# Performance work log

Hardware: AMD Instinct MI355X
Metric: run time of the kernel (lower is better)

## Reference

```python
import jax, jax.numpy as jnp
import numpy as np

COMMITMENT_COST = 0.25


def setup_inputs() -> dict:
    key = jax.random.key(0)
    k1, k2 = jax.random.split(key)
    x = jax.random.normal(k1, (65536, 256), dtype=jnp.float32)
    codebook = jax.random.normal(k2, (1024, 256), dtype=jnp.float32)
    return {"x": x, "codebook": codebook}


def reference(x, codebook):
    # Flatten to [N, D] (already 2D here).
    flat = x.reshape(-1, codebook.shape[1])
    # Squared euclidean distances [N, K]; argmin matches torch.cdist argmin.
    x2 = jnp.sum(flat * flat, axis=1, keepdims=True)          # [N, 1]
    c2 = jnp.sum(codebook * codebook, axis=1)                  # [K]
    d2 = x2 - 2.0 * (flat @ codebook.T) + c2[None, :]          # [N, K]
    encoding_indices = jnp.argmin(d2, axis=1)                  # [N]
    quantized = codebook[encoding_indices]                     # [N, D]
    # VQ loss + commitment loss
    vq_loss = jnp.mean((jax.lax.stop_gradient(quantized) - flat) ** 2)
    commitment_loss = jnp.mean((quantized - jax.lax.stop_gradient(flat)) ** 2)
    quantization_loss = vq_loss + COMMITMENT_COST * commitment_loss
    # Straight-through estimator
    quantized_st = flat + jax.lax.stop_gradient(quantized - flat)
    quantized_st = quantized_st.reshape(x.shape)
    return quantized_st, quantization_loss, encoding_indices
```

## Files before the change

kernel.cpp:

```cpp
#include <hip/hip_runtime.h>

#define NROWS 65536
#define DDIM  256
#define KCODES 1024
#define MARGIN 0.05f
#define TIE_WINDOW 8.0e-5
#define FLAGCAP 8192

typedef __attribute__((ext_vector_type(8))) short bf16x8;
typedef __attribute__((ext_vector_type(4))) float f32x4;

union F4 { float4 v; float f[4]; };

__device__ __forceinline__ unsigned bf16rne(float f) {
    unsigned u = __float_as_uint(f);
    return (u + 0x7fffu + ((u >> 16) & 1u)) >> 16;
}
__device__ __forceinline__ float bf16tof(unsigned h) {
    return __uint_as_float(h << 16);
}

__global__ __launch_bounds__(64) void c2_kernel(const float* __restrict__ cb,
                                                float* __restrict__ c2f,
                                                double* __restrict__ c2d,
                                                int* __restrict__ cnt) {
    const int c = blockIdx.x, lane = threadIdx.x;
    if (c == 0 && lane == 0) cnt[0] = 0;
    F4 v; v.v = reinterpret_cast<const float4*>(cb + (size_t)c * DDIM)[lane];
    double s = (double)v.f[0] * v.f[0] + (double)v.f[1] * v.f[1]
             + (double)v.f[2] * v.f[2] + (double)v.f[3] * v.f[3];
    #pragma unroll
    for (int off = 32; off; off >>= 1) s += __shfl_xor(s, off);
    if (lane == 0) { c2d[c] = s; c2f[c] = (float)s; }
}

__global__ __launch_bounds__(256) void prep_frags(const float* __restrict__ cb,
                                                  unsigned short* __restrict__ fh,
                                                  unsigned short* __restrict__ fl) {
    int t = blockIdx.x * 256 + threadIdx.x;
    int j0   = (t & 1) * 4;
    int lane = (t >> 1) & 63;
    int ks   = (t >> 7) & 7;
    int ntg  = t >> 10;
    int c = ntg * 16 + (lane & 15);
    int k = ks * 32 + (lane >> 4) * 8 + j0;
    F4 v; v.v = *reinterpret_cast<const float4*>(cb + (size_t)c * DDIM + k);
    unsigned h0 = bf16rne(v.f[0]), h1 = bf16rne(v.f[1]),
             h2 = bf16rne(v.f[2]), h3 = bf16rne(v.f[3]);
    unsigned l0 = bf16rne(v.f[0] - bf16tof(h0)), l1 = bf16rne(v.f[1] - bf16tof(h1)),
             l2 = bf16rne(v.f[2] - bf16tof(h2)), l3 = bf16rne(v.f[3] - bf16tof(h3));
    unsigned* ph = reinterpret_cast<unsigned*>(fh + (size_t)t * 4);
    unsigned* pl = reinterpret_cast<unsigned*>(fl + (size_t)t * 4);
    ph[0] = h0 | (h1 << 16); ph[1] = h2 | (h3 << 16);
    pl[0] = l0 | (l1 << 16); pl[1] = l2 | (l3 << 16);
}

__global__ __launch_bounds__(512) void vqmfma(const float* __restrict__ x,
                                              const float* __restrict__ cb,
                                              const unsigned short* __restrict__ fbh,
                                              const unsigned short* __restrict__ fbl,
                                              const float* __restrict__ c2f,
                                              float* __restrict__ out_idx,
                                              int* __restrict__ flaglist,
                                              int* __restrict__ cnt,
                                              float* __restrict__ out_q,
                                              float* __restrict__ rowsq,
                                              int fuse) {
    __shared__ bf16x8 lds_ah[1024];
    __shared__ bf16x8 lds_al[1024];
    __shared__ float  lds_c2[KCODES];
    __shared__ float  m_b1[256]; __shared__ float m_b2[256]; __shared__ int m_i1[256];
    __shared__ float  x2s[32];
    __shared__ int    sbest[32];

    const int tid  = threadIdx.x;
    const int w    = tid >> 6;
    const int lane = tid & 63;
    const int row0 = blockIdx.x * 32;

    #pragma unroll
    for (int q = 0; q < 2; q++) lds_c2[q * 512 + tid] = c2f[q * 512 + tid];

    {
        const float4* gx = reinterpret_cast<const float4*>(x + (size_t)row0 * DDIM);
        unsigned* pah = reinterpret_cast<unsigned*>(lds_ah);
        unsigned* pal = reinterpret_cast<unsigned*>(lds_al);
        #pragma unroll
        for (int jj = 0; jj < 4; jj++) {
            int flat4 = jj * 512 + tid;
            int r = flat4 >> 6;
            int k = (flat4 & 63) * 4;
            F4 v; v.v = gx[flat4];
            float sq = v.f[0]*v.f[0] + v.f[1]*v.f[1] + v.f[2]*v.f[2] + v.f[3]*v.f[3];
            #pragma unroll
            for (int off = 32; off; off >>= 1) sq += __shfl_xor(sq, off);
            if (lane == 0) x2s[r] = sq;
            int rt = r >> 4, row = r & 15;
            int ks = k >> 5, gg = (k >> 3) & 3, j0 = k & 7;
            int laneS = gg * 16 + row;
            int u32i = ((((rt * 8 + ks) * 64 + laneS) * 8 + j0) >> 1);
            unsigned h0 = bf16rne(v.f[0]), h1 = bf16rne(v.f[1]),
                     h2 = bf16rne(v.f[2]), h3 = bf16rne(v.f[3]);
            pah[u32i]     = h0 | (h1 << 16);
            pah[u32i + 1] = h2 | (h3 << 16);
            unsigned l0 = bf16rne(v.f[0] - bf16tof(h0)), l1 = bf16rne(v.f[1] - bf16tof(h1)),
                     l2 = bf16rne(v.f[2] - bf16tof(h2)), l3 = bf16rne(v.f[3] - bf16tof(h3));
            pal[u32i]     = l0 | (l1 << 16);
            pal[u32i + 1] = l2 | (l3 << 16);
        }
    }
    __syncthreads();

    float bestv[8], secv[8]; int besti[8];
    #pragma unroll
    for (int e = 0; e < 8; e++) { bestv[e] = 1e30f; secv[e] = 1e30f; besti[e] = 0; }

    const bf16x8* Bh = reinterpret_cast<const bf16x8*>(fbh);
    const bf16x8* Bl = reinterpret_cast<const bf16x8*>(fbl);

    for (int cc = 0; cc < KCODES; cc += 256) {
        f32x4 acc[2][2];
        #pragma unroll
        for (int rt = 0; rt < 2; rt++)
            #pragma unroll
            for (int nt = 0; nt < 2; nt++) acc[rt][nt] = (f32x4){0.f, 0.f, 0.f, 0.f};

        const int ntg0 = (cc >> 4) + w * 2;
        const bf16x8* b0h = Bh + (size_t)(ntg0 * 8) * 64 + lane;
        const bf16x8* b0l = Bl + (size_t)(ntg0 * 8) * 64 + lane;
        const bf16x8* b1h = b0h + 8 * 64;
        const bf16x8* b1l = b0l + 8 * 64;
        const bf16x8* a0  = &lds_ah[lane];
        const bf16x8* a1  = &lds_ah[8 * 64 + lane];
        const bf16x8* a0l = &lds_al[lane];
        const bf16x8* a1l = &lds_al[8 * 64 + lane];

        #pragma unroll
        for (int ks = 0; ks < 8; ks++) {
            bf16x8 ah0 = a0[ks * 64],  ah1 = a1[ks * 64];
            bf16x8 al0 = a0l[ks * 64], al1 = a1l[ks * 64];
            bf16x8 bh0 = b0h[ks * 64], bl0 = b0l[ks * 64];
            bf16x8 bh1 = b1h[ks * 64], bl1 = b1l[ks * 64];
            acc[0][0] = __builtin_amdgcn_mfma_f32_16x16x32_bf16(ah0, bh0, acc[0][0], 0, 0, 0);
            acc[1][0] = __builtin_amdgcn_mfma_f32_16x16x32_bf16(ah1, bh0, acc[1][0], 0, 0, 0);
            acc[0][1] = __builtin_amdgcn_mfma_f32_16x16x32_bf16(ah0, bh1, acc[0][1], 0, 0, 0);
            acc[1][1] = __builtin_amdgcn_mfma_f32_16x16x32_bf16(ah1, bh1, acc[1][1], 0, 0, 0);
            acc[0][0] = __builtin_amdgcn_mfma_f32_16x16x32_bf16(ah0, bl0, acc[0][0], 0, 0, 0);
            acc[1][0] = __builtin_amdgcn_mfma_f32_16x16x32_bf16(ah1, bl0, acc[1][0], 0, 0, 0);
            acc[0][1] = __builtin_amdgcn_mfma_f32_16x16x32_bf16(ah0, bl1, acc[0][1], 0, 0, 0);
            acc[1][1] = __builtin_amdgcn_mfma_f32_16x16x32_bf16(ah1, bl1, acc[1][1], 0, 0, 0);
            acc[0][0] = __builtin_amdgcn_mfma_f32_16x16x32_bf16(al0, bh0, acc[0][0], 0, 0, 0);
            acc[1][0] = __builtin_amdgcn_mfma_f32_16x16x32_bf16(al1, bh0, acc[1][0], 0, 0, 0);
            acc[0][1] = __builtin_amdgcn_mfma_f32_16x16x32_bf16(al0, bh1, acc[0][1], 0, 0, 0);
            acc[1][1] = __builtin_amdgcn_mfma_f32_16x16x32_bf16(al1, bh1, acc[1][1], 0, 0, 0);
        }
        #pragma unroll
        for (int nt = 0; nt < 2; nt++) {
            int c = cc + w * 32 + nt * 16 + (lane & 15);
            float c2v = lds_c2[c];
            #pragma unroll
            for (int rt = 0; rt < 2; rt++)
                #pragma unroll
                for (int reg = 0; reg < 4; reg++) {
                    float s = __fmaf_rn(-2.f, acc[rt][nt][reg], c2v);
                    int e = rt * 4 + reg;
                    if (s < bestv[e]) { secv[e] = bestv[e]; bestv[e] = s; besti[e] = c; }
                    else if (s < secv[e]) secv[e] = s;
                }
        }
    }

    #pragma unroll
    for (int e = 0; e < 8; e++) {
        float b1 = bestv[e]; int i1 = besti[e]; float b2 = secv[e];
        #pragma unroll
        for (int off = 8; off; off >>= 1) {
            float o1 = __shfl_xor(b1, off, 16);
            int   oi = __shfl_xor(i1, off, 16);
            float o2 = __shfl_xor(b2, off, 16);
            if (o1 < b1 || (o1 == b1 && oi < i1)) { b2 = fminf(b1, o2); b1 = o1; i1 = oi; }
            else                                  { b2 = fminf(o1, b2); }
        }
        if ((lane & 15) == 0) {
            int rt = e >> 2, reg = e & 3;
            int rib = rt * 16 + (lane >> 4) * 4 + reg;
            m_b1[w * 32 + rib] = b1; m_i1[w * 32 + rib] = i1; m_b2[w * 32 + rib] = b2;
        }
    }
    __syncthreads();

    if (tid < 32) {
        float b1 = m_b1[tid]; int i1 = m_i1[tid]; float b2 = m_b2[tid];
        #pragma unroll
        for (int ww = 1; ww < 8; ww++) {
            float o1 = m_b1[ww * 32 + tid]; int oi = m_i1[ww * 32 + tid];
            float o2 = m_b2[ww * 32 + tid];
            if (o1 < b1 || (o1 == b1 && oi < i1)) { b2 = fminf(b1, o2); b1 = o1; i1 = oi; }
            else                                  { b2 = fminf(o1, b2); }
        }
        out_idx[row0 + tid] = (float)i1;
        sbest[tid] = i1;
        if (fuse) rowsq[row0 + tid] = b1 + x2s[tid];
        if (b2 - b1 < MARGIN) {
            int slot = atomicAdd(cnt, 1);
            if (slot < FLAGCAP) flaglist[slot] = row0 + tid;
        }
    }
    if (fuse) {
        __syncthreads();
        int r  = tid >> 4;
        int d0 = (tid & 15) * 16;
        int bi = sbest[r];
        const float4* gq = reinterpret_cast<const float4*>(cb + (size_t)bi * DDIM + d0);
        float4* go = reinterpret_cast<float4*>(out_q + (size_t)(row0 + r) * DDIM + d0);
        go[0] = gq[0]; go[1] = gq[1]; go[2] = gq[2]; go[3] = gq[3];
    }
}

__global__ __launch_bounds__(256) void refine_f(const float* __restrict__ x,
                                                const float* __restrict__ cb,
                                                const double* __restrict__ c2d,
                                                const int* __restrict__ flaglist,
                                                const int* __restrict__ cnt,
                                                float* __restrict__ out_idx,
                                                float* __restrict__ out_q,
                                                float* __restrict__ rowsq) {
    __shared__ double xs[DDIM];
    __shared__ double redd[256];
    __shared__ int    redi[256];
    const int tid = threadIdx.x;
    const int n = min(cnt[0], FLAGCAP);

    for (int fi = blockIdx.x; fi < n; fi += gridDim.x) {
        const int row = flaglist[fi];
        const double xv = (double)x[(size_t)row * DDIM + tid];
        xs[tid] = xv;
        redd[tid] = xv * xv;
        __syncthreads();
        for (int off = 128; off; off >>= 1) {
            if (tid < off) redd[tid] += redd[tid + off];
            __syncthreads();
        }
        const double x2 = redd[0];
        __syncthreads();

        double d2v[4];
        #pragma unroll
        for (int j = 0; j < 4; j++) {
            const int c = tid + 256 * j;
            const float* cp = cb + (size_t)c * DDIM;
            double dot = 0.0;
            for (int d = 0; d < DDIM; d += 4) {
                F4 cv; cv.v = *reinterpret_cast<const float4*>(cp + d);
                dot += xs[d+0]*(double)cv.f[0] + xs[d+1]*(double)cv.f[1]
                     + xs[d+2]*(double)cv.f[2] + xs[d+3]*(double)cv.f[3];
            }
            d2v[j] = x2 - 2.0 * dot + c2d[c];
        }
        double mv = fmin(fmin(d2v[0], d2v[1]), fmin(d2v[2], d2v[3]));
        redd[tid] = mv;
        __syncthreads();
        for (int off = 128; off; off >>= 1) {
            if (tid < off) redd[tid] = fmin(redd[tid], redd[tid + off]);
            __syncthreads();
        }
        const double thr = redd[0] + TIE_WINDOW;
        __syncthreads();
        int ci = 0x7fffffff;
        #pragma unroll
        for (int j = 0; j < 4; j++)
            if (d2v[j] <= thr) ci = min(ci, tid + 256 * j);
        redi[tid] = ci;
        __syncthreads();
        for (int off = 128; off; off >>= 1) {
            if (tid < off) redi[tid] = min(redi[tid], redi[tid + off]);
            __syncthreads();
        }
        const int widx = redi[0];
        __syncthreads();
        const float qn = cb[(size_t)widx * DDIM + tid];
        out_q[(size_t)row * DDIM + tid] = qn;
        const double dn = (double)qn - xv;
        redd[tid] = dn * dn;
        __syncthreads();
        for (int off = 128; off; off >>= 1) {
            if (tid < off) redd[tid] += redd[tid + off];
            __syncthreads();
        }
        if (tid == 0) {
            rowsq[row]   = (float)redd[0];
            out_idx[row] = (float)widx;
        }
        __syncthreads();
    }
}

__global__ __launch_bounds__(256) void refine_kernel(const float* __restrict__ x,
                                                     const float* __restrict__ cb,
                                                     const double* __restrict__ c2d,
                                                     const int* __restrict__ flaglist,
                                                     const int* __restrict__ cnt,
                                                     float* __restrict__ out_idx) {
    __shared__ double xs[DDIM];
    __shared__ double redd[256];
    __shared__ int    redi[256];
    const int tid = threadIdx.x;
    const int n = min(cnt[0], FLAGCAP);
    for (int fi = blockIdx.x; fi < n; fi += gridDim.x) {
        const int row = flaglist[fi];
        const double xv = (double)x[(size_t)row * DDIM + tid];
        xs[tid] = xv;
        redd[tid] = xv * xv;
        __syncthreads();
        for (int off = 128; off; off >>= 1) {
            if (tid < off) redd[tid] += redd[tid + off];
            __syncthreads();
        }
        const double x2 = redd[0];
        __syncthreads();
        double d2v[4];
        #pragma unroll
        for (int j = 0; j < 4; j++) {
            const int c = tid + 256 * j;
            const float* cp = cb + (size_t)c * DDIM;
            double dot = 0.0;
            for (int d = 0; d < DDIM; d += 4) {
                F4 cv; cv.v = *reinterpret_cast<const float4*>(cp + d);
                dot += xs[d+0]*(double)cv.f[0] + xs[d+1]*(double)cv.f[1]
                     + xs[d+2]*(double)cv.f[2] + xs[d+3]*(double)cv.f[3];
            }
            d2v[j] = x2 - 2.0 * dot + c2d[c];
        }
        double mv = fmin(fmin(d2v[0], d2v[1]), fmin(d2v[2], d2v[3]));
        redd[tid] = mv;
        __syncthreads();
        for (int off = 128; off; off >>= 1) {
            if (tid < off) redd[tid] = fmin(redd[tid], redd[tid + off]);
            __syncthreads();
        }
        const double thr = redd[0] + TIE_WINDOW;
        __syncthreads();
        int ci = 0x7fffffff;
        #pragma unroll
        for (int j = 0; j < 4; j++)
            if (d2v[j] <= thr) ci = min(ci, tid + 256 * j);
        redi[tid] = ci;
        __syncthreads();
        for (int off = 128; off; off >>= 1) {
            if (tid < off) redi[tid] = min(redi[tid], redi[tid + off]);
            __syncthreads();
        }
        if (tid == 0) out_idx[row] = (float)redi[0];
        __syncthreads();
    }
}

__global__ __launch_bounds__(256) void gather_kernel(const float* __restrict__ x,
                                                     const float* __restrict__ cb,
                                                     const float* __restrict__ out_idx,
                                                     float* __restrict__ out_q,
                                                     float* __restrict__ partial) {
    __shared__ float wsum[4];
    const int tid = threadIdx.x;
    const int row = blockIdx.x * 32 + (tid >> 3);
    const int d0  = (tid & 7) * 32;
    const int bi  = (int)out_idx[row];
    const float4* gq = reinterpret_cast<const float4*>(cb + (size_t)bi * DDIM + d0);
    const float4* gx = reinterpret_cast<const float4*>(x + (size_t)row * DDIM + d0);
    float4* go = reinterpret_cast<float4*>(out_q + (size_t)row * DDIM + d0);
    float sq = 0.f;
    #pragma unroll
    for (int j = 0; j < 8; j++) {
        F4 q, xv; q.v = gq[j]; xv.v = gx[j];
        go[j] = q.v;
        #pragma unroll
        for (int t = 0; t < 4; t++) { float d = q.f[t] - xv.f[t]; sq += d * d; }
    }
    #pragma unroll
    for (int off = 32; off; off >>= 1) sq += __shfl_down(sq, off);
    if ((tid & 63) == 0) wsum[tid >> 6] = sq;
    __syncthreads();
    if (tid == 0) partial[blockIdx.x] = wsum[0] + wsum[1] + wsum[2] + wsum[3];
}

__global__ __launch_bounds__(1024) void loss_rowsq(const float* __restrict__ rowsq,
                                                   float* __restrict__ out_loss) {
    __shared__ float w[16];
    float s = 0.f;
    for (int j = threadIdx.x; j < NROWS; j += 1024) s += rowsq[j];
    #pragma unroll
    for (int off = 32; off; off >>= 1) s += __shfl_down(s, off);
    if ((threadIdx.x & 63) == 0) w[threadIdx.x >> 6] = s;
    __syncthreads();
    if (threadIdx.x == 0) {
        float tot = 0.f;
        #pragma unroll
        for (int i = 0; i < 16; i++) tot += w[i];
        out_loss[0] = 1.25f * tot / 16777216.f;
    }
}

__global__ __launch_bounds__(256) void loss_kernel(const float* __restrict__ partial,
                                                   float* __restrict__ out_loss) {
    __shared__ float w[4];
    float s = 0.f;
    for (int j = threadIdx.x; j < 2048; j += 256) s += partial[j];
    #pragma unroll
    for (int off = 32; off; off >>= 1) s += __shfl_down(s, off);
    if ((threadIdx.x & 63) == 0) w[threadIdx.x >> 6] = s;
    __syncthreads();
    if (threadIdx.x == 0)
        out_loss[0] = 1.25f * (w[0] + w[1] + w[2] + w[3]) / 16777216.f;
}

extern "C" void kernel_launch(void* const* d_in, const int* in_sizes, int n_in,
                              void* d_out, int out_size, void* d_ws, size_t ws_size,
                              hipStream_t stream) {
    const float* x  = (const float*)d_in[0];
    const float* cb = (const float*)d_in[1];
    float* out      = (float*)d_out;
    float* out_q    = out;
    float* out_loss = out + 16777216;
    float* out_idx  = out + 16777217;

    char* wsp = (char*)d_ws;
    float*  ws_c2f     = (float*) (wsp +      0);
    double* ws_c2d     = (double*)(wsp +   4096);
    int*    ws_flag    = (int*)   (wsp +  12288);
    int*    ws_cnt     = (int*)   (wsp +  45056);
    float*  ws_rowsq   = (float*) (wsp +  45120);
    float*  ws_partial = (float*) (wsp + 307264);
    unsigned short* ws_fbh = (unsigned short*)(wsp + 315456);
    unsigned short* ws_fbl = ws_fbh + 262144;
    const size_t NEED = 1364032;

    c2_kernel<<<KCODES, 64, 0, stream>>>(cb, ws_c2f, ws_c2d, ws_cnt);

    if (ws_size >= NEED) {
        prep_frags<<<256, 256, 0, stream>>>(cb, ws_fbh, ws_fbl);
        vqmfma<<<NROWS / 32, 512, 0, stream>>>(x, cb, ws_fbh, ws_fbl, ws_c2f,
                                               out_idx, ws_flag, ws_cnt,
                                               out_q, ws_rowsq, 1);
        refine_f<<<256, 256, 0, stream>>>(x, cb, ws_c2d, ws_flag, ws_cnt,
                                          out_idx, out_q, ws_rowsq);
        loss_rowsq<<<1, 1024, 0, stream>>>(ws_rowsq, out_loss);
    } else {
        unsigned short* fbh = (unsigned short*)d_out;
        unsigned short* fbl = fbh + 262144;
        prep_frags<<<256, 256, 0, stream>>>(cb, fbh, fbl);
        vqmfma<<<NROWS / 32, 512, 0, stream>>>(x, cb, fbh, fbl, ws_c2f,
                                               out_idx, ws_flag, ws_cnt,
                                               out_q, ws_rowsq, 0);
        refine_kernel<<<256, 256, 0, stream>>>(x, cb, ws_c2d, ws_flag, ws_cnt, out_idx);
        gather_kernel<<<NROWS / 32, 256, 0, stream>>>(x, cb, out_idx, out_q, ws_partial);
        loss_kernel<<<1, 256, 0, stream>>>(ws_partial, out_loss);
    }
}
```

Baseline: 251.5 us.

## Restructure VQ MFMA kernel: register-resident x tiles, LDS double-buffered codebook

Each block now handles 128 rows instead of 32. Each wave keeps its own 16 rows of x as split-bf16 fragments in registers and sweeps the whole codebook, 32 codes at a time. Codebook fragments are streamed into double-buffered LDS with global_load_lds, so a block reads the codebook 4x less often per row and the fetch overlaps the MFMAs. Because each wave sees every code for its rows, the cross-wave argmin merge through shared memory goes away. The costs are a __syncthreads on each of the 32 steps, higher register pressure, and fewer blocks (512) to spread across the CUs.

```diff
diff --git a/kernel.cpp b/kernel.cpp
--- a/kernel.cpp
+++ b/kernel.cpp
@@ -3,6 +3,7 @@
 #define NROWS 65536
 #define DDIM  256
 #define KCODES 1024
+#define BROWS 128
 #define MARGIN 0.05f
 #define TIE_WINDOW 8.0e-5
 #define FLAGCAP 8192
@@ -11,6 +12,7 @@
 typedef __attribute__((ext_vector_type(4))) float f32x4;
 
 union F4 { float4 v; float f[4]; };
+union BF8 { bf16x8 v; unsigned short s[8]; };
 
 __device__ __forceinline__ unsigned bf16rne(float f) {
     unsigned u = __float_as_uint(f);
@@ -18,6 +20,11 @@
 }
 __device__ __forceinline__ float bf16tof(unsigned h) {
     return __uint_as_float(h << 16);
+}
+__device__ __forceinline__ void load_lds16(const void* g, void* l) {
+    __builtin_amdgcn_global_load_lds(
+        (const __attribute__((address_space(1))) void*)g,
+        (__attribute__((address_space(3))) void*)l, 16, 0, 0);
 }
 
 __global__ __launch_bounds__(64) void c2_kernel(const float* __restrict__ cb,
@@ -66,112 +73,113 @@
                                               float* __restrict__ out_q,
                                               float* __restrict__ rowsq,
                                               int fuse) {
-    __shared__ bf16x8 lds_ah[1024];
-    __shared__ bf16x8 lds_al[1024];
+    __shared__ bf16x8 bufH[2][1024];
+    __shared__ bf16x8 bufL[2][1024];
     __shared__ float  lds_c2[KCODES];
-    __shared__ float  m_b1[256]; __shared__ float m_b2[256]; __shared__ int m_i1[256];
-    __shared__ float  x2s[32];
-    __shared__ int    sbest[32];
+    __shared__ float  x2s[BROWS];
+    __shared__ int    sbest[BROWS];
 
     const int tid  = threadIdx.x;
     const int w    = tid >> 6;
     const int lane = tid & 63;
-    const int row0 = blockIdx.x * 32;
-
-    #pragma unroll
-    for (int q = 0; q < 2; q++) lds_c2[q * 512 + tid] = c2f[q * 512 + tid];
+    const int row0 = blockIdx.x * BROWS;
+
+    lds_c2[tid] = c2f[tid];
+    lds_c2[512 + tid] = c2f[512 + tid];
 
     {
-        const float4* gx = reinterpret_cast<const float4*>(x + (size_t)row0 * DDIM);
-        unsigned* pah = reinterpret_cast<unsigned*>(lds_ah);
-        unsigned* pal = reinterpret_cast<unsigned*>(lds_al);
-        #pragma unroll
-        for (int jj = 0; jj < 4; jj++) {
-            int flat4 = jj * 512 + tid;
-            int r = flat4 >> 6;
-            int k = (flat4 & 63) * 4;
-            F4 v; v.v = gx[flat4];
-            float sq = v.f[0]*v.f[0] + v.f[1]*v.f[1] + v.f[2]*v.f[2] + v.f[3]*v.f[3];
+        const char* gh = (const char*)fbh + w * 2048 + (size_t)lane * 16;
+        const char* gl = (const char*)fbl + w * 2048 + (size_t)lane * 16;
+        char* lh = (char*)&bufH[0][0] + w * 2048;
+        char* ll = (char*)&bufL[0][0] + w * 2048;
+        load_lds16(gh,        lh);
+        load_lds16(gh + 1024, lh + 1024);
+        load_lds16(gl,        ll);
+        load_lds16(gl + 1024, ll + 1024);
+    }
+
+    bf16x8 Ah[8], Al[8];
+    {
+        const int arow = row0 + w * 16 + (lane & 15);
+        const int k0   = (lane >> 4) * 8;
+        float sq = 0.f;
+        #pragma unroll
+        for (int ks = 0; ks < 8; ks++) {
+            F4 v0, v1;
+            v0.v = *reinterpret_cast<const float4*>(x + (size_t)arow * DDIM + ks * 32 + k0);
+            v1.v = *reinterpret_cast<const float4*>(x + (size_t)arow * DDIM + ks * 32 + k0 + 4);
+            float f[8] = {v0.f[0], v0.f[1], v0.f[2], v0.f[3],
+                          v1.f[0], v1.f[1], v1.f[2], v1.f[3]};
+            BF8 hh, ll;
             #pragma unroll
-            for (int off = 32; off; off >>= 1) sq += __shfl_xor(sq, off);
-            if (lane == 0) x2s[r] = sq;
-            int rt = r >> 4, row = r & 15;
-            int ks = k >> 5, gg = (k >> 3) & 3, j0 = k & 7;
-            int laneS = gg * 16 + row;
-            int u32i = ((((rt * 8 + ks) * 64 + laneS) * 8 + j0) >> 1);
-            unsigned h0 = bf16rne(v.f[0]), h1 = bf16rne(v.f[1]),
-                     h2 = bf16rne(v.f[2]), h3 = bf16rne(v.f[3]);
-            pah[u32i]     = h0 | (h1 << 16);
-            pah[u32i + 1] = h2 | (h3 << 16);
-            unsigned l0 = bf16rne(v.f[0] - bf16tof(h0)), l1 = bf16rne(v.f[1] - bf16tof(h1)),
-                     l2 = bf16rne(v.f[2] - bf16tof(h2)), l3 = bf16rne(v.f[3] - bf16tof(h3));
-            pal[u32i]     = l0 | (l1 << 16);
-            pal[u32i + 1] = l2 | (l3 << 16);
-        }
-    }
+            for (int j = 0; j < 8; j++) {
+                sq += f[j] * f[j];
+                unsigned h = bf16rne(f[j]);
+                hh.s[j] = (unsigned short)h;
+                ll.s[j] = (unsigned short)bf16rne(f[j] - bf16tof(h));
+            }
+            Ah[ks] = hh.v; Al[ks] = ll.v;
+        }
+        sq += __shfl_xor(sq, 16);
+        sq += __shfl_xor(sq, 32);
+        if (lane < 16) x2s[w * 16 + lane] = sq;
+    }
+
+    float bestv[4], secv[4]; int besti[4];
+    #pragma unroll
+    for (int e = 0; e < 4; e++) { bestv[e] = 1e30f; secv[e] = 1e30f; besti[e] = 0; }
+
     __syncthreads();
 
-    float bestv[8], secv[8]; int besti[8];
-    #pragma unroll
-    for (int e = 0; e < 8; e++) { bestv[e] = 1e30f; secv[e] = 1e30f; besti[e] = 0; }
-
-    const bf16x8* Bh = reinterpret_cast<const bf16x8*>(fbh);
-    const bf16x8* Bl = reinterpret_cast<const bf16x8*>(fbl);
-
-    for (int cc = 0; cc < KCODES; cc += 256) {
-        f32x4 acc[2][2];
-        #pragma unroll
-        for (int rt = 0; rt < 2; rt++)
+    int cur = 0;
+    for (int t = 0; t < 32; t++) {
+        if (t < 31) {
+            const char* gh = (const char*)fbh + (size_t)(t + 1) * 16384 + w * 2048 + (size_t)lane * 16;
+            const char* gl = (const char*)fbl + (size_t)(t + 1) * 16384 + w * 2048 + (size_t)lane * 16;
+            char* lh = (char*)&bufH[cur ^ 1][0] + w * 2048;
+            char* ll = (char*)&bufL[cur ^ 1][0] + w * 2048;
+            load_lds16(gh,        lh);
+            load_lds16(gh + 1024, lh + 1024);
+            load_lds16(gl,        ll);
+            load_lds16(gl + 1024, ll + 1024);
+        }
+        const bf16x8* BH = &bufH[cur][0];
+        const bf16x8* BL = &bufL[cur][0];
+        f32x4 acc0 = (f32x4){0.f, 0.f, 0.f, 0.f};
+        f32x4 acc1 = (f32x4){0.f, 0.f, 0.f, 0.f};
+        #pragma unroll
+        for (int ks = 0; ks < 8; ks++) {
+            bf16x8 bh0 = BH[ks * 64 + lane];
+            bf16x8 bh1 = BH[(8 + ks) * 64 + lane];
+            bf16x8 bl0 = BL[ks * 64 + lane];
+            bf16x8 bl1 = BL[(8 + ks) * 64 + lane];
+            acc0 = __builtin_amdgcn_mfma_f32_16x16x32_bf16(Ah[ks], bh0, acc0, 0, 0, 0);
+            acc1 = __builtin_amdgcn_mfma_f32_16x16x32_bf16(Ah[ks], bh1, acc1, 0, 0, 0);
+            acc0 = __builtin_amdgcn_mfma_f32_16x16x32_bf16(Ah[ks], bl0, acc0, 0, 0, 0);
+            acc1 = __builtin_amdgcn_mfma_f32_16x16x32_bf16(Ah[ks], bl1, acc1, 0, 0, 0);
+            acc0 = __builtin_amdgcn_mfma_f32_16x16x32_bf16(Al[ks], bh0, acc0, 0, 0, 0);
+            acc1 = __builtin_amdgcn_mfma_f32_16x16x32_bf16(Al[ks], bh1, acc1, 0, 0, 0);
+        }
+        {
+            int cbase = t * 32 + (lane & 15);
+            float c2v0 = lds_c2[cbase];
+            float c2v1 = lds_c2[cbase + 16];
             #pragma unroll
-            for (int nt = 0; nt < 2; nt++) acc[rt][nt] = (f32x4){0.f, 0.f, 0.f, 0.f};
-
-        const int ntg0 = (cc >> 4) + w * 2;
-        const bf16x8* b0h = Bh + (size_t)(ntg0 * 8) * 64 + lane;
-        const bf16x8* b0l = Bl + (size_t)(ntg0 * 8) * 64 + lane;
-        const bf16x8* b1h = b0h + 8 * 64;
-        const bf16x8* b1l = b0l + 8 * 64;
-        const bf16x8* a0  = &lds_ah[lane];
-        const bf16x8* a1  = &lds_ah[8 * 64 + lane];
-        const bf16x8* a0l = &lds_al[lane];
-        const bf16x8* a1l = &lds_al[8 * 64 + lane];
-
-        #pragma unroll
-        for (int ks = 0; ks < 8; ks++) {
-            bf16x8 ah0 = a0[ks * 64],  ah1 = a1[ks * 64];
-            bf16x8 al0 = a0l[ks * 64], al1 = a1l[ks * 64];
-            bf16x8 bh0 = b0h[ks * 64], bl0 = b0l[ks * 64];
-            bf16x8 bh1 = b1h[ks * 64], bl1 = b1l[ks * 64];
-            acc[0][0] = __builtin_amdgcn_mfma_f32_16x16x32_bf16(ah0, bh0, acc[0][0], 0, 0, 0);
-            acc[1][0] = __builtin_amdgcn_mfma_f32_16x16x32_bf16(ah1, bh0, acc[1][0], 0, 0, 0);
-            acc[0][1] = __builtin_amdgcn_mfma_f32_16x16x32_bf16(ah0, bh1, acc[0][1], 0, 0, 0);
-            acc[1][1] = __builtin_amdgcn_mfma_f32_16x16x32_bf16(ah1, bh1, acc[1][1], 0, 0, 0);
-            acc[0][0] = __builtin_amdgcn_mfma_f32_16x16x32_bf16(ah0, bl0, acc[0][0], 0, 0, 0);
-            acc[1][0] = __builtin_amdgcn_mfma_f32_16x16x32_bf16(ah1, bl0, acc[1][0], 0, 0, 0);
-            acc[0][1] = __builtin_amdgcn_mfma_f32_16x16x32_bf16(ah0, bl1, acc[0][1], 0, 0, 0);
-            acc[1][1] = __builtin_amdgcn_mfma_f32_16x16x32_bf16(ah1, bl1, acc[1][1], 0, 0, 0);
-            acc[0][0] = __builtin_amdgcn_mfma_f32_16x16x32_bf16(al0, bh0, acc[0][0], 0, 0, 0);
-            acc[1][0] = __builtin_amdgcn_mfma_f32_16x16x32_bf16(al1, bh0, acc[1][0], 0, 0, 0);
-            acc[0][1] = __builtin_amdgcn_mfma_f32_16x16x32_bf16(al0, bh1, acc[0][1], 0, 0, 0);
-            acc[1][1] = __builtin_amdgcn_mfma_f32_16x16x32_bf16(al1, bh1, acc[1][1], 0, 0, 0);
-        }
-        #pragma unroll
-        for (int nt = 0; nt < 2; nt++) {
-            int c = cc + w * 32 + nt * 16 + (lane & 15);
-            float c2v = lds_c2[c];
-            #pragma unroll
-            for (int rt = 0; rt < 2; rt++)
-                #pragma unroll
-                for (int reg = 0; reg < 4; reg++) {
-                    float s = __fmaf_rn(-2.f, acc[rt][nt][reg], c2v);
-                    int e = rt * 4 + reg;
-                    if (s < bestv[e]) { secv[e] = bestv[e]; bestv[e] = s; besti[e] = c; }
-                    else if (s < secv[e]) secv[e] = s;
-                }
-        }
-    }
-
-    #pragma unroll
-    for (int e = 0; e < 8; e++) {
+            for (int reg = 0; reg < 4; reg++) {
+                float s0 = __fmaf_rn(-2.f, acc0[reg], c2v0);
+                if (s0 < bestv[reg]) { secv[reg] = bestv[reg]; bestv[reg] = s0; besti[reg] = cbase; }
+                else if (s0 < secv[reg]) secv[reg] = s0;
+                float s1 = __fmaf_rn(-2.f, acc1[reg], c2v1);
+                if (s1 < bestv[reg]) { secv[reg] = bestv[reg]; bestv[reg] = s1; besti[reg] = cbase + 16; }
+                else if (s1 < secv[reg]) secv[reg] = s1;
+            }
+        }
+        __syncthreads();
+        cur ^= 1;
+    }
+
+    #pragma unroll
+    for (int e = 0; e < 4; e++) {
         float b1 = bestv[e]; int i1 = besti[e]; float b2 = secv[e];
         #pragma unroll
         for (int off = 8; off; off >>= 1) {
@@ -182,38 +190,25 @@
             else                                  { b2 = fminf(o1, b2); }
         }
         if ((lane & 15) == 0) {
-            int rt = e >> 2, reg = e & 3;
-            int rib = rt * 16 + (lane >> 4) * 4 + reg;
-            m_b1[w * 32 + rib] = b1; m_i1[w * 32 + rib] = i1; m_b2[w * 32 + rib] = b2;
-        }
-    }
-    __syncthreads();
-
-    if (tid < 32) {
-        float b1 = m_b1[tid]; int i1 = m_i1[tid]; float b2 = m_b2[tid];
-        #pragma unroll
-        for (int ww = 1; ww < 8; ww++) {
-            float o1 = m_b1[ww * 32 + tid]; int oi = m_i1[ww * 32 + tid];
-            float o2 = m_b2[ww * 32 + tid];
-            if (o1 < b1 || (o1 == b1 && oi < i1)) { b2 = fminf(b1, o2); b1 = o1; i1 = oi; }
-            else                                  { b2 = fminf(o1, b2); }
-        }
-        out_idx[row0 + tid] = (float)i1;
-        sbest[tid] = i1;
-        if (fuse) rowsq[row0 + tid] = b1 + x2s[tid];
-        if (b2 - b1 < MARGIN) {
-            int slot = atomicAdd(cnt, 1);
-            if (slot < FLAGCAP) flaglist[slot] = row0 + tid;
+            int rib = w * 16 + (lane >> 4) * 4 + e;
+            sbest[rib] = i1;
+            out_idx[row0 + rib] = (float)i1;
+            if (fuse) rowsq[row0 + rib] = b1 + x2s[rib];
+            if (b2 - b1 < MARGIN) {
+                int slot = atomicAdd(cnt, 1);
+                if (slot < FLAGCAP) flaglist[slot] = row0 + rib;
+            }
         }
     }
     if (fuse) {
         __syncthreads();
-        int r  = tid >> 4;
-        int d0 = (tid & 15) * 16;
+        int r  = tid >> 2;
+        int d0 = (tid & 3) * 64;
         int bi = sbest[r];
         const float4* gq = reinterpret_cast<const float4*>(cb + (size_t)bi * DDIM + d0);
         float4* go = reinterpret_cast<float4*>(out_q + (size_t)(row0 + r) * DDIM + d0);
-        go[0] = gq[0]; go[1] = gq[1]; go[2] = gq[2]; go[3] = gq[3];
+        #pragma unroll
+        for (int j = 0; j < 16; j++) go[j] = gq[j];
     }
 }
 
@@ -438,9 +433,9 @@
 
     if (ws_size >= NEED) {
         prep_frags<<<256, 256, 0, stream>>>(cb, ws_fbh, ws_fbl);
-        vqmfma<<<NROWS / 32, 512, 0, stream>>>(x, cb, ws_fbh, ws_fbl, ws_c2f,
-                                               out_idx, ws_flag, ws_cnt,
-                                               out_q, ws_rowsq, 1);
+        vqmfma<<<NROWS / BROWS, 512, 0, stream>>>(x, cb, ws_fbh, ws_fbl, ws_c2f,
+                                                  out_idx, ws_flag, ws_cnt,
+                                                  out_q, ws_rowsq, 1);
         refine_f<<<256, 256, 0, stream>>>(x, cb, ws_c2d, ws_flag, ws_cnt,
                                           out_idx, out_q, ws_rowsq);
         loss_rowsq<<<1, 1024, 0, stream>>>(ws_rowsq, out_loss);
@@ -448,9 +443,9 @@
         unsigned short* fbh = (unsigned short*)d_out;
         unsigned short* fbl = fbh + 262144;
         prep_frags<<<256, 256, 0, stream>>>(cb, fbh, fbl);
-        vqmfma<<<NROWS / 32, 512, 0, stream>>>(x, cb, fbh, fbl, ws_c2f,
-                                               out_idx, ws_flag, ws_cnt,
-                                               out_q, ws_rowsq, 0);
+        vqmfma<<<NROWS / BROWS, 512, 0, stream>>>(x, cb, fbh, fbl, ws_c2f,
+                                                  out_idx, ws_flag, ws_cnt,
+                                                  out_q, ws_rowsq, 0);
         refine_kernel<<<256, 256, 0, stream>>>(x, cb, ws_c2d, ws_flag, ws_cnt, out_idx);
         gather_kernel<<<NROWS / 32, 256, 0, stream>>>(x, cb, out_idx, out_q, ws_partial);
         loss_kernel<<<1, 256, 0, stream>>>(ws_partial, out_loss);
```

Result: slower. 274.2 us (+9.0%).
